# Kernel tuning notes

Measured on AMD Instinct MI355X. Metric: run time of the kernel, lower is better.

## Reference

```python
import jax, jax.numpy as jnp
import numpy as np
from jax import lax

OUT_BINS = 256  # final time slice [:, :, :, :256, :]

def setup_inputs() -> dict:
    key = jax.random.key(0)
    k1, k2 = jax.random.split(key)
    B, X, Y, T = 8, 128, 128, 256
    data = jax.random.uniform(k1, (B, X, Y, T, 1), dtype=jnp.float32)
    irf = jax.random.uniform(k2, (B, 1, 1, T, 1), dtype=jnp.float32)
    return {"data": data, "irf": irf}

def _full_conv1d(sig_b, ker_b):
    # sig_b: [X, Y, T], ker_b: [T]. Full (polynomial) convolution along time,
    # which is exactly stride-1 VALID conv3d_transpose with a [1,1,T,1,1] kernel.
    X, Y, T = sig_b.shape
    lhs = sig_b.reshape(X * Y, 1, T)              # [N, C=1, W]
    rhs = ker_b[::-1].reshape(1, 1, T)            # flip -> true convolution
    out = lax.conv_general_dilated(lhs, rhs, window_strides=(1,), padding=[(T - 1, T - 1)])
    return out.reshape(X, Y, 2 * T - 1)

def reference(data, irf):
    B, X, Y, T, _ = data.shape
    k = irf.reshape(B, T)
    # per-sample kernel normalization: k / max(k)
    k = k / jnp.max(k, axis=1, keepdims=True)
    out = jax.vmap(_full_conv1d)(data[..., 0], k)  # [B, X, Y, 2T-1]
    return out[..., :OUT_BINS][..., None]          # [B, X, Y, 256, 1]
```

## Files before the change

kernel.cpp:

```cpp
#include <hip/hip_runtime.h>


typedef __attribute__((ext_vector_type(8))) short short8;
typedef __attribute__((ext_vector_type(4))) float floatx4;

#define T_BINS 256
#define PIX_PER_B (128 * 128)

__device__ inline unsigned short f2bf(float f) {
    unsigned int u = __float_as_uint(f);
    u += 0x7fffu + ((u >> 16) & 1u);
    return (unsigned short)(u >> 16);
}

__global__ __launch_bounds__(256) void build_W(const float* __restrict__ irf,
                                               unsigned short* __restrict__ W) {
    __shared__ float red[256];
    __shared__ float knorm[256];
    const int b = blockIdx.x;
    const int t = threadIdx.x;
    float v = irf[b * T_BINS + t];
    red[t] = v;
    __syncthreads();
    for (int s = 128; s > 0; s >>= 1) {
        if (t < s) red[t] = fmaxf(red[t], red[t + s]);
        __syncthreads();
    }
    knorm[t] = v / red[0];
    __syncthreads();
    unsigned short* Wb = W + b * 8192;
#pragma unroll
    for (int i = 0; i < 32; i++) {
        int e = i * 256 + t;
        int d  = e >> 9;
        int np = (e >> 5) & 15;
        int kl = e & 31;
        int idx = 16 * d + np - kl;
        Wb[e] = (idx >= 0) ? f2bf(knorm[idx]) : (unsigned short)0;
    }
}

__device__ inline short8 cvt_a(float4 lo, float4 hi) {
    short8 a;
    a[0] = (short)f2bf(lo.x); a[1] = (short)f2bf(lo.y);
    a[2] = (short)f2bf(lo.z); a[3] = (short)f2bf(lo.w);
    a[4] = (short)f2bf(hi.x); a[5] = (short)f2bf(hi.y);
    a[6] = (short)f2bf(hi.z); a[7] = (short)f2bf(hi.w);
    return a;
}

__global__ __launch_bounds__(256, 2) void conv_gemm(const float* __restrict__ data,
                                                    const unsigned short* __restrict__ W,
                                                    float* __restrict__ out) {
    const int b = blockIdx.x >> 8;
    const int mt = blockIdx.x & 255;
    const int t = threadIdx.x;
    const int w = t >> 6;
    const int l = t & 63;
    const int lq = l >> 4;
    const int lm = l & 15;

    const int row = mt * 64 + w * 16 + lm;
    const float* Arow = data + ((size_t)b * PIX_PER_B + row) * T_BINS;
    const unsigned short* Wd = W + b * 8192;

    short8 bd[16];
#pragma unroll
    for (int d = 0; d < 16; d++)
        bd[d] = *(const short8*)(Wd + d * 512 + lm * 32 + lq * 8);

    float4 araw[8][2];
#pragma unroll
    for (int kk = 0; kk < 8; kk++) {
        araw[kk][0] = *(const float4*)(Arow + kk * 32 + lq * 8);
        araw[kk][1] = *(const float4*)(Arow + kk * 32 + lq * 8 + 4);
    }
    __builtin_amdgcn_sched_barrier(0);

    floatx4 acc[16];
#pragma unroll
    for (int j = 0; j < 16; j++) acc[j] = (floatx4){0.f, 0.f, 0.f, 0.f};

#pragma unroll
    for (int kk = 0; kk < 8; kk++) {
        short8 a = cvt_a(araw[kk][0], araw[kk][1]);
#pragma unroll
        for (int j = 2 * kk; j < 16; j++) {
            acc[j] = __builtin_amdgcn_mfma_f32_16x16x32_bf16(bd[j - 2 * kk], a,
                                                             acc[j], 0, 0, 0);
        }
    }

    float* Orow = out + ((size_t)b * PIX_PER_B + mt * 64 + w * 16 + lm) * T_BINS;
#pragma unroll
    for (int j = 0; j < 16; j++) {
        *reinterpret_cast<floatx4*>(Orow + 16 * j + 4 * lq) = acc[j];
    }
}

extern "C" void kernel_launch(void* const* d_in, const int* in_sizes, int n_in,
                              void* d_out, int out_size, void* d_ws, size_t ws_size,
                              hipStream_t stream) {
    const float* data = (const float*)d_in[0];
    const float* irf  = (const float*)d_in[1];
    float* outp = (float*)d_out;
    unsigned short* W = (unsigned short*)d_ws;

    build_W<<<8, 256, 0, stream>>>(irf, W);
    conv_gemm<<<2048, 256, 0, stream>>>(data, W, outp);
}
```

Measured before the change: 244.3 us.

## Stage Toeplitz weights in LDS and stream output tiles to cut registers

Moves the per-batch Toeplitz weight matrix from registers into shared memory and reads fragments per MFMA. The loop is reordered so each output tile is accumulated and stored right away instead of holding 16 accumulators, and the A loads are double-buffered four chunks ahead. Together these lower register pressure so the launch bound can target 4 blocks per CU, to hide memory latency on this bandwidth-bound kernel. The cost is repeated LDS reads of B fragments plus a block barrier.

```diff
diff --git a/kernel.cpp b/kernel.cpp
--- a/kernel.cpp
+++ b/kernel.cpp
@@ -49,7 +49,7 @@
     return a;
 }
 
-__global__ __launch_bounds__(256, 2) void conv_gemm(const float* __restrict__ data,
+__global__ __launch_bounds__(256, 4) void conv_gemm(const float* __restrict__ data,
                                                     const unsigned short* __restrict__ W,
                                                     float* __restrict__ out) {
     const int b = blockIdx.x >> 8;
@@ -60,41 +60,53 @@
     const int lq = l >> 4;
     const int lm = l & 15;
 
+    __shared__ unsigned short Bs[8192];
+    {
+        const short8* src = (const short8*)(W + b * 8192);
+        short8* dst = (short8*)Bs;
+#pragma unroll
+        for (int i = 0; i < 4; i++)
+            dst[i * 256 + t] = src[i * 256 + t];
+    }
+
     const int row = mt * 64 + w * 16 + lm;
     const float* Arow = data + ((size_t)b * PIX_PER_B + row) * T_BINS;
-    const unsigned short* Wd = W + b * 8192;
 
-    short8 bd[16];
+    float4 fbuf[4][2];
 #pragma unroll
-    for (int d = 0; d < 16; d++)
-        bd[d] = *(const short8*)(Wd + d * 512 + lm * 32 + lq * 8);
+    for (int kk = 0; kk < 4; kk++) {
+        fbuf[kk][0] = *(const float4*)(Arow + kk * 32 + lq * 8);
+        fbuf[kk][1] = *(const float4*)(Arow + kk * 32 + lq * 8 + 4);
+    }
 
-    float4 araw[8][2];
-#pragma unroll
-    for (int kk = 0; kk < 8; kk++) {
-        araw[kk][0] = *(const float4*)(Arow + kk * 32 + lq * 8);
-        araw[kk][1] = *(const float4*)(Arow + kk * 32 + lq * 8 + 4);
-    }
-    __builtin_amdgcn_sched_barrier(0);
+    __syncthreads();
 
-    floatx4 acc[16];
-#pragma unroll
-    for (int j = 0; j < 16; j++) acc[j] = (floatx4){0.f, 0.f, 0.f, 0.f};
+    float* Orow = out + ((size_t)b * PIX_PER_B + row) * T_BINS;
+    const unsigned short* BsLane = Bs + lm * 32 + lq * 8;
+
+    short8 af[8];
 
 #pragma unroll
     for (int kk = 0; kk < 8; kk++) {
-        short8 a = cvt_a(araw[kk][0], araw[kk][1]);
+        const int cb = kk & 3;
+        af[kk] = cvt_a(fbuf[cb][0], fbuf[cb][1]);
+        if (kk + 4 < 8) {
+            fbuf[cb][0] = *(const float4*)(Arow + (kk + 4) * 32 + lq * 8);
+            fbuf[cb][1] = *(const float4*)(Arow + (kk + 4) * 32 + lq * 8 + 4);
+        }
 #pragma unroll
-        for (int j = 2 * kk; j < 16; j++) {
-            acc[j] = __builtin_amdgcn_mfma_f32_16x16x32_bf16(bd[j - 2 * kk], a,
-                                                             acc[j], 0, 0, 0);
+        for (int jo = 0; jo < 2; jo++) {
+            const int j = 2 * kk + jo;
+            floatx4 acc = (floatx4){0.f, 0.f, 0.f, 0.f};
+#pragma unroll
+            for (int k2 = 0; k2 <= kk; k2++) {
+                const int d = j - 2 * k2;
+                short8 bf = *(const short8*)(BsLane + d * 512);
+                acc = __builtin_amdgcn_mfma_f32_16x16x32_bf16(bf, af[k2],
+                                                              acc, 0, 0, 0);
+            }
+            *reinterpret_cast<floatx4*>(Orow + 16 * j + 4 * lq) = acc;
         }
-    }
-
-    float* Orow = out + ((size_t)b * PIX_PER_B + mt * 64 + w * 16 + lm) * T_BINS;
-#pragma unroll
-    for (int j = 0; j < 16; j++) {
-        *reinterpret_cast<floatx4*>(Orow + 16 * j + 4 * lq) = acc[j];
     }
 }
 
```

New measurement: 243.8 us. Within noise of the previous version (-0.2%).

## Stage Toeplitz weights in LDS and process two tiles per block with prefetch

Applied to the files above, without the earlier changes.

Banded weight fragments are now loaded once per block into shared memory via global_load_lds instead of held as 16 register fragments. Each block handles two 64-row tiles and prefetches the second tile's inputs while the first tile's MFMAs run. Accumulation is restructured to one accumulator per output chunk, and launch bounds rise to 4 waves per SIMD for occupancy. The W layout is permuted to match the LDS read pattern. The cost is extra LDS reads per MFMA and a block-wide sync.

```diff
diff --git a/kernel.cpp b/kernel.cpp
--- a/kernel.cpp
+++ b/kernel.cpp
@@ -6,6 +6,13 @@
 
 #define T_BINS 256
 #define PIX_PER_B (128 * 128)
+
+typedef __attribute__((address_space(3))) void lds_void;
+typedef __attribute__((address_space(1))) const void gbl_void;
+
+__device__ __forceinline__ void gload_lds16(const void* g, void* l) {
+    __builtin_amdgcn_global_load_lds((gbl_void*)g, (lds_void*)l, 16, 0, 0);
+}
 
 __device__ inline unsigned short f2bf(float f) {
     unsigned int u = __float_as_uint(f);
@@ -33,8 +40,10 @@
     for (int i = 0; i < 32; i++) {
         int e = i * 256 + t;
         int d  = e >> 9;
-        int np = (e >> 5) & 15;
-        int kl = e & 31;
+        int lq = (e >> 7) & 3;
+        int np = (e >> 3) & 15;
+        int k8 = e & 7;
+        int kl = lq * 8 + k8;
         int idx = 16 * d + np - kl;
         Wb[e] = (idx >= 0) ? f2bf(knorm[idx]) : (unsigned short)0;
     }
@@ -49,52 +58,78 @@
     return a;
 }
 
-__global__ __launch_bounds__(256, 2) void conv_gemm(const float* __restrict__ data,
+__global__ __launch_bounds__(256, 4) void conv_gemm(const float* __restrict__ data,
                                                     const unsigned short* __restrict__ W,
                                                     float* __restrict__ out) {
-    const int b = blockIdx.x >> 8;
-    const int mt = blockIdx.x & 255;
+    __shared__ alignas(16) unsigned short Bs[8192];
+
+    const int b = blockIdx.x >> 7;
+    const int bm = blockIdx.x & 127;
     const int t = threadIdx.x;
     const int w = t >> 6;
     const int l = t & 63;
     const int lq = l >> 4;
     const int lm = l & 15;
 
-    const int row = mt * 64 + w * 16 + lm;
-    const float* Arow = data + ((size_t)b * PIX_PER_B + row) * T_BINS;
-    const unsigned short* Wd = W + b * 8192;
+    const unsigned short* Wb = W + b * 8192;
+#pragma unroll
+    for (int i = 0; i < 4; i++)
+        gload_lds16(Wb + (i * 256 + t) * 8,
+                    (unsigned char*)Bs + i * 4096 + w * 1024);
 
-    short8 bd[16];
-#pragma unroll
-    for (int d = 0; d < 16; d++)
-        bd[d] = *(const short8*)(Wd + d * 512 + lm * 32 + lq * 8);
+    const int mt0 = bm, mt1 = bm + 128;
+    const float* A0 = data + ((size_t)b * PIX_PER_B + mt0 * 64 + w * 16 + lm) * T_BINS + lq * 8;
+    const float* A1 = data + ((size_t)b * PIX_PER_B + mt1 * 64 + w * 16 + lm) * T_BINS + lq * 8;
+    float* O0 = out + ((size_t)b * PIX_PER_B + mt0 * 64 + w * 16 + lm) * T_BINS;
+    float* O1 = out + ((size_t)b * PIX_PER_B + mt1 * 64 + w * 16 + lm) * T_BINS;
+    const unsigned short* BsL = Bs + l * 8;
 
-    float4 araw[8][2];
+    float4 raw[8][2];
+    short8 af[8];
+
 #pragma unroll
     for (int kk = 0; kk < 8; kk++) {
-        araw[kk][0] = *(const float4*)(Arow + kk * 32 + lq * 8);
-        araw[kk][1] = *(const float4*)(Arow + kk * 32 + lq * 8 + 4);
+        raw[kk][0] = *(const float4*)(A0 + kk * 32);
+        raw[kk][1] = *(const float4*)(A0 + kk * 32 + 4);
     }
     __builtin_amdgcn_sched_barrier(0);
 
-    floatx4 acc[16];
 #pragma unroll
-    for (int j = 0; j < 16; j++) acc[j] = (floatx4){0.f, 0.f, 0.f, 0.f};
+    for (int kk = 0; kk < 8; kk++) af[kk] = cvt_a(raw[kk][0], raw[kk][1]);
+
+    __syncthreads();
 
 #pragma unroll
     for (int kk = 0; kk < 8; kk++) {
-        short8 a = cvt_a(araw[kk][0], araw[kk][1]);
-#pragma unroll
-        for (int j = 2 * kk; j < 16; j++) {
-            acc[j] = __builtin_amdgcn_mfma_f32_16x16x32_bf16(bd[j - 2 * kk], a,
-                                                             acc[j], 0, 0, 0);
-        }
+        raw[kk][0] = *(const float4*)(A1 + kk * 32);
+        raw[kk][1] = *(const float4*)(A1 + kk * 32 + 4);
     }
+    __builtin_amdgcn_sched_barrier(0);
 
-    float* Orow = out + ((size_t)b * PIX_PER_B + mt * 64 + w * 16 + lm) * T_BINS;
 #pragma unroll
     for (int j = 0; j < 16; j++) {
-        *reinterpret_cast<floatx4*>(Orow + 16 * j + 4 * lq) = acc[j];
+        floatx4 acc = (floatx4){0.f, 0.f, 0.f, 0.f};
+#pragma unroll
+        for (int k2 = 0; k2 <= (j >> 1); k2++) {
+            short8 bf = *(const short8*)(BsL + (j - 2 * k2) * 512);
+            acc = __builtin_amdgcn_mfma_f32_16x16x32_bf16(bf, af[k2], acc, 0, 0, 0);
+        }
+        *reinterpret_cast<floatx4*>(O0 + 16 * j + 4 * lq) = acc;
+    }
+    __builtin_amdgcn_sched_barrier(0);
+
+#pragma unroll
+    for (int kk = 0; kk < 8; kk++) af[kk] = cvt_a(raw[kk][0], raw[kk][1]);
+
+#pragma unroll
+    for (int j = 0; j < 16; j++) {
+        floatx4 acc = (floatx4){0.f, 0.f, 0.f, 0.f};
+#pragma unroll
+        for (int k2 = 0; k2 <= (j >> 1); k2++) {
+            short8 bf = *(const short8*)(BsL + (j - 2 * k2) * 512);
+            acc = __builtin_amdgcn_mfma_f32_16x16x32_bf16(bf, af[k2], acc, 0, 0, 0);
+        }
+        *reinterpret_cast<floatx4*>(O1 + 16 * j + 4 * lq) = acc;
     }
 }
 
@@ -107,5 +142,5 @@
     unsigned short* W = (unsigned short*)d_ws;
 
     build_W<<<8, 256, 0, stream>>>(irf, W);
-    conv_gemm<<<2048, 256, 0, stream>>>(data, W, outp);
+    conv_gemm<<<1024, 256, 0, stream>>>(data, W, outp);
 }
```

Result: slower. 257.7 us (+5.5%).
